# Kernel tuning notes

Measured on AMD Instinct MI355X. Metric: run time of the kernel, lower is better.

Reference implementation:

```python
import jax, jax.numpy as jnp
import numpy as np

D = 1024
H = 16
DH = D // H
FF = 4096
EPS = 1e-6


def setup_inputs() -> dict:
    key = jax.random.key(0)
    ks = jax.random.split(key, 8)
    s = 1.0 / np.sqrt(D)
    return {
        "x": jax.random.normal(ks[0], (2, 2048, D), jnp.float32),
        # attention projections stored [in, out] (math equals torch Linear x @ W.T)
        "w_q": jax.random.normal(ks[1], (D, D), jnp.float32) * s,
        "w_k": jax.random.normal(ks[2], (D, D), jnp.float32) * s,
        "w_v": jax.random.normal(ks[3], (D, D), jnp.float32) * s,
        "w_o": jax.random.normal(ks[4], (D, D), jnp.float32) * s,
        "w1": jax.random.normal(ks[5], (D, FF), jnp.float32) * s,
        "b1": jnp.zeros((FF,), jnp.float32),
        "w2": jax.random.normal(ks[6], (FF, D), jnp.float32) * (1.0 / np.sqrt(FF)),
        "b2": jnp.zeros((D,), jnp.float32),
        "g1": jnp.ones((D,), jnp.float32),
        "be1": jnp.zeros((D,), jnp.float32),
        "g2": jnp.ones((D,), jnp.float32),
        "be2": jnp.zeros((D,), jnp.float32),
    }


def _layernorm(x, gamma, beta):
    # torch .std() uses Bessel correction (ddof=1); note std+eps, not var+eps
    mean = jnp.mean(x, axis=-1, keepdims=True)
    std = jnp.std(x, axis=-1, keepdims=True, ddof=1)
    return gamma * (x - mean) / (std + EPS) + beta


def _attention(h, w_q, w_k, w_v, w_o):
    B, S, _ = h.shape
    q = (h @ w_q).reshape(B, S, H, DH)
    k = (h @ w_k).reshape(B, S, H, DH)
    v = (h @ w_v).reshape(B, S, H, DH)
    scores = jnp.einsum('bqhd,bkhd->bhqk', q, k) / np.sqrt(DH)  # [B,H,S,S]
    attn = jax.nn.softmax(scores, axis=-1)
    out = jnp.einsum('bhqk,bkhd->bqhd', attn, v).reshape(B, S, D)
    return out @ w_o


def reference(x, w_q, w_k, w_v, w_o, w1, b1, w2, b2, g1, be1, g2, be2):
    # pre-norm residual 1: self-attention (dropout=0 / eval)
    x = x + _attention(_layernorm(x, g1, be1), w_q, w_k, w_v, w_o)
    # pre-norm residual 2: FFN
    h = _layernorm(x, g2, be2)
    x = x + (jax.nn.relu(h @ w1 + b1) @ w2 + b2)
    return x
```

## Files before the change

kernel.cpp:

```cpp
#include <hip/hip_runtime.h>


typedef _Float16 half8 __attribute__((ext_vector_type(8)));
typedef _Float16 half4 __attribute__((ext_vector_type(4)));
typedef float floatx4 __attribute__((ext_vector_type(4)));

__device__ __forceinline__ void async16(const void* g, void* l) {
    __builtin_amdgcn_global_load_lds((const __attribute__((address_space(1))) unsigned int*)g,
                                     (__attribute__((address_space(3))) unsigned int*)l,
                                     16, 0, 0);
}

__global__ __launch_bounds__(256) void ln_kernel(const float* __restrict__ x,
                                                 const float* __restrict__ g,
                                                 const float* __restrict__ be,
                                                 _Float16* __restrict__ out) {
    int row = blockIdx.x;
    int tid = threadIdx.x;
    floatx4 v = ((const floatx4*)(x + (size_t)row * 1024))[tid];
    float s = 0.f, ss = 0.f;
#pragma unroll
    for (int i = 0; i < 4; i++) { s += v[i]; ss += v[i] * v[i]; }
#pragma unroll
    for (int off = 1; off < 64; off <<= 1) {
        s += __shfl_xor(s, off);
        ss += __shfl_xor(ss, off);
    }
    __shared__ float sm[8];
    int wave = tid >> 6, lane = tid & 63;
    if (lane == 0) { sm[wave] = s; sm[wave + 4] = ss; }
    __syncthreads();
    s = sm[0] + sm[1] + sm[2] + sm[3];
    ss = sm[4] + sm[5] + sm[6] + sm[7];
    float mean = s * (1.f / 1024.f);
    float var = (ss - s * mean) * (1.f / 1023.f);
    float rs = 1.f / (sqrtf(fmaxf(var, 0.f)) + 1e-6f);
    floatx4 gv = ((const floatx4*)g)[tid];
    floatx4 bv = ((const floatx4*)be)[tid];
    half4 o;
#pragma unroll
    for (int i = 0; i < 4; i++) o[i] = (_Float16)(gv[i] * (v[i] - mean) * rs + bv[i]);
    ((half4*)(out + (size_t)row * 1024))[tid] = o;
}

__global__ __launch_bounds__(256) void convt_kernel(const float* __restrict__ W, int ldW,
                                                    _Float16* __restrict__ WT, int Kr,
                                                    float scale) {
    __shared__ float t[64][65];
    int n0 = blockIdx.x * 64, k0 = blockIdx.y * 64;
    int tid = threadIdx.x;
    int r = tid >> 4, c4 = (tid & 15) * 4;
#pragma unroll
    for (int p = 0; p < 4; p++) {
        floatx4 v = *(const floatx4*)(W + (size_t)(k0 + r + p * 16) * ldW + n0 + c4);
#pragma unroll
        for (int j = 0; j < 4; j++) t[c4 + j][r + p * 16] = v[j];
    }
    __syncthreads();
#pragma unroll
    for (int p = 0; p < 4; p++) {
        int rr = r + p * 16;
        half4 o;
#pragma unroll
        for (int j = 0; j < 4; j++) o[j] = (_Float16)(t[rr][c4 + j] * scale);
        *(half4*)(WT + (size_t)(n0 + rr) * Kr + k0 + c4) = o;
    }
}

__global__ __launch_bounds__(256) void transv_kernel(const _Float16* __restrict__ V, int ldv,
                                                     _Float16* __restrict__ Vt) {
    __shared__ _Float16 t[64][72];
    int t0 = blockIdx.x * 64, d0 = blockIdx.y * 64;
    int tid = threadIdx.x;
#pragma unroll
    for (int i = 0; i < 2; i++) {
        int v = tid + i * 256;
        int r = v >> 3, c = (v & 7) * 8;
        half8 vv = *(const half8*)(V + (size_t)(t0 + r) * ldv + d0 + c);
#pragma unroll
        for (int j = 0; j < 8; j++) t[c + j][r] = vv[j];
    }
    __syncthreads();
    int bh = (t0 >> 11) * 16 + (d0 >> 6);
    int sbase = t0 & 2047;
#pragma unroll
    for (int i = 0; i < 2; i++) {
        int v = tid + i * 256;
        int r = v >> 3, c = (v & 7) * 8;
        half8 o = *(const half8*)&t[r][c];
        *(half8*)(Vt + ((size_t)bh * 64 + r) * 2048 + sbase + c) = o;
    }
}

__global__ __launch_bounds__(256) void gemm_t(const _Float16* __restrict__ A, int lda,
                                              const _Float16* __restrict__ BT,
                                              const float* __restrict__ bias,
                                              const float* res, void* Cout,
                                              int N, int K, int relu_flag, int out_fp16) {
    __shared__ _Float16 As[64 * 64];
    __shared__ _Float16 Bs[128 * 64];
    int tid = threadIdx.x;
    int wave = tid >> 6, lane = tid & 63, quad = lane >> 4, l15 = lane & 15;
    int bm = blockIdx.y * 64, bn = blockIdx.x * 128;
    int wr = (wave & 1) * 32, wc = (wave >> 1) * 64;
    int lrow = lane >> 3, lch = lane & 7;

    floatx4 acc[2][4];
#pragma unroll
    for (int im = 0; im < 2; im++)
#pragma unroll
        for (int in = 0; in < 4; in++)
#pragma unroll
            for (int r = 0; r < 4; r++) acc[im][in][r] = 0.f;

    for (int k0 = 0; k0 < K; k0 += 64) {
        __syncthreads();
#pragma unroll
        for (int ia = 0; ia < 2; ia++) {
            int g = 2 * wave + ia;
            int row = g * 8 + lrow;
            int ch = lch ^ (row & 7);
            async16(A + (size_t)(bm + row) * lda + k0 + ch * 8, &As[g * 512]);
        }
#pragma unroll
        for (int ib = 0; ib < 4; ib++) {
            int g = 4 * wave + ib;
            int row = g * 8 + lrow;
            int ch = lch ^ (row & 7);
            async16(BT + (size_t)(bn + row) * K + k0 + ch * 8, &Bs[g * 512]);
        }
        __syncthreads();

        half8 af[2][2], bf[4][2];
#pragma unroll
        for (int kk = 0; kk < 2; kk++) {
#pragma unroll
            for (int im = 0; im < 2; im++) {
                int m = wr + im * 16 + l15;
                af[im][kk] = *(const half8*)&As[m * 64 + ((((kk << 2) | quad) ^ (m & 7)) << 3)];
            }
#pragma unroll
            for (int in = 0; in < 4; in++) {
                int n = wc + in * 16 + l15;
                bf[in][kk] = *(const half8*)&Bs[n * 64 + ((((kk << 2) | quad) ^ (n & 7)) << 3)];
            }
        }
#pragma unroll
        for (int kk = 0; kk < 2; kk++)
#pragma unroll
            for (int im = 0; im < 2; im++)
#pragma unroll
                for (int in = 0; in < 4; in++)
                    acc[im][in] = __builtin_amdgcn_mfma_f32_16x16x32_f16(af[im][kk], bf[in][kk],
                                                                         acc[im][in], 0, 0, 0);
    }
#pragma unroll
    for (int im = 0; im < 2; im++)
#pragma unroll
        for (int in = 0; in < 4; in++)
#pragma unroll
            for (int r = 0; r < 4; r++) {
                int row = bm + wr + im * 16 + quad * 4 + r;
                int col = bn + wc + in * 16 + l15;
                float val = acc[im][in][r];
                if (bias) val += bias[col];
                if (relu_flag) val = fmaxf(val, 0.f);
                if (res) val += res[(size_t)row * N + col];
                if (out_fp16) ((_Float16*)Cout)[(size_t)row * N + col] = (_Float16)val;
                else          ((float*)Cout)[(size_t)row * N + col] = val;
            }
}

__global__ __launch_bounds__(256) void attn_kernel(const _Float16* Q,
                                                   const _Float16* __restrict__ K,
                                                   const _Float16* __restrict__ Vt,
                                                   _Float16* O, int ld) {
    __shared__ _Float16 Qs[64 * 64];
    __shared__ _Float16 KVs[2][2][64 * 64];
    int qt = blockIdx.x, bh = blockIdx.y;
    int b = bh >> 4, h = bh & 15;
    int col0 = h * 64, tbase = b * 2048;
    int tid = threadIdx.x;
    int wave = tid >> 6, lane = tid & 63, quad = lane >> 4, l15 = lane & 15;
    int lrow = lane >> 3, lch = lane & 7;

#pragma unroll
    for (int i = 0; i < 2; i++) {
        int g = 2 * wave + i;
        int row = g * 8 + lrow;
        int ch = lch ^ (row & 7);
        async16(Q + (size_t)(tbase + qt * 64 + row) * ld + col0 + ch * 8, &Qs[g * 512]);
        async16(K + (size_t)(tbase + row) * ld + col0 + ch * 8, &KVs[0][0][g * 512]);
        async16(Vt + ((size_t)bh * 64 + row) * 2048 + ch * 8, &KVs[0][1][g * 512]);
    }
    __syncthreads();

    int rowq = 16 * wave + l15;
    half8 bq[2];
#pragma unroll
    for (int kk = 0; kk < 2; kk++)
        bq[kk] = *(const half8*)&Qs[rowq * 64 + ((((kk << 2) | quad) ^ (rowq & 7)) << 3)];

    floatx4 o_acc[4];
#pragma unroll
    for (int im = 0; im < 4; im++)
#pragma unroll
        for (int r = 0; r < 4; r++) o_acc[im][r] = 0.f;
    float m_i = -1e30f, l_i = 0.f;

    for (int kt = 0; kt < 32; kt++) {
        if (kt) __syncthreads();
        if (kt + 1 < 32) {
            int nb = (kt + 1) & 1;
#pragma unroll
            for (int i = 0; i < 2; i++) {
                int g = 2 * wave + i;
                int row = g * 8 + lrow;
                int ch = lch ^ (row & 7);
                async16(K + (size_t)(tbase + (kt + 1) * 64 + row) * ld + col0 + ch * 8,
                        &KVs[nb][0][g * 512]);
                async16(Vt + ((size_t)bh * 64 + row) * 2048 + (kt + 1) * 64 + ch * 8,
                        &KVs[nb][1][g * 512]);
            }
        }
        const _Float16* Ks = KVs[kt & 1][0];
        const _Float16* Vs = KVs[kt & 1][1];

        floatx4 s_acc[4];
#pragma unroll
        for (int jn = 0; jn < 4; jn++)
#pragma unroll
            for (int r = 0; r < 4; r++) s_acc[jn][r] = 0.f;
#pragma unroll
        for (int jn = 0; jn < 4; jn++) {
            int rowk = 16 * jn + l15;
#pragma unroll
            for (int kk = 0; kk < 2; kk++) {
                half8 ak = *(const half8*)&Ks[rowk * 64 + ((((kk << 2) | quad) ^ (rowk & 7)) << 3)];
                s_acc[jn] = __builtin_amdgcn_mfma_f32_16x16x32_f16(ak, bq[kk], s_acc[jn], 0, 0, 0);
            }
        }

        float mx = -1e30f;
#pragma unroll
        for (int jn = 0; jn < 4; jn++)
#pragma unroll
            for (int r = 0; r < 4; r++) mx = fmaxf(mx, s_acc[jn][r]);
        mx = fmaxf(mx, __shfl_xor(mx, 16));
        mx = fmaxf(mx, __shfl_xor(mx, 32));
        float mnew = fmaxf(m_i, mx);
        float dd = m_i - mnew;
        float alpha = (dd < -60.f) ? 0.f : __expf(dd);
        m_i = mnew;

        float sum = 0.f;
#pragma unroll
        for (int jn = 0; jn < 4; jn++)
#pragma unroll
            for (int r = 0; r < 4; r++) {
                float d2 = s_acc[jn][r] - mnew;
                float p = (d2 < -60.f) ? 0.f : __expf(d2);
                s_acc[jn][r] = p;
                sum += p;
            }
        sum += __shfl_xor(sum, 16);
        sum += __shfl_xor(sum, 32);
        l_i = l_i * alpha + sum;

        half4 pb[4];
#pragma unroll
        for (int jn = 0; jn < 4; jn++)
#pragma unroll
            for (int r = 0; r < 4; r++) pb[jn][r] = (_Float16)s_acc[jn][r];

#pragma unroll
        for (int im = 0; im < 4; im++)
#pragma unroll
            for (int r = 0; r < 4; r++) o_acc[im][r] *= alpha;
#pragma unroll
        for (int im = 0; im < 4; im++) {
            int rowv = 16 * im + l15;
#pragma unroll
            for (int ks = 0; ks < 4; ks++) {
                int off = rowv * 128 + ((((2 * ks) | (quad >> 1)) ^ (rowv & 7)) << 4) + (quad & 1) * 8;
                half4 av = *(const half4*)((const char*)Vs + off);
                o_acc[im] = __builtin_amdgcn_mfma_f32_16x16x16f16(av, pb[ks], o_acc[im], 0, 0, 0);
            }
        }
    }

    float rl = 1.f / l_i;
#pragma unroll
    for (int im = 0; im < 4; im++) {
        half4 o;
#pragma unroll
        for (int r = 0; r < 4; r++) o[r] = (_Float16)(o_acc[im][r] * rl);
        *(half4*)&O[(size_t)(tbase + qt * 64 + wave * 16 + l15) * ld + col0 + im * 16 + quad * 4] = o;
    }
}

extern "C" void kernel_launch(void* const* d_in, const int* in_sizes, int n_in,
                              void* d_out, int out_size, void* d_ws, size_t ws_size,
                              hipStream_t stream) {
    const float* x   = (const float*)d_in[0];
    const float* wq  = (const float*)d_in[1];
    const float* wk  = (const float*)d_in[2];
    const float* wv  = (const float*)d_in[3];
    const float* wo  = (const float*)d_in[4];
    const float* w1  = (const float*)d_in[5];
    const float* b1  = (const float*)d_in[6];
    const float* w2  = (const float*)d_in[7];
    const float* b2  = (const float*)d_in[8];
    const float* g1  = (const float*)d_in[9];
    const float* be1 = (const float*)d_in[10];
    const float* g2  = (const float*)d_in[11];
    const float* be2 = (const float*)d_in[12];

    const size_t M1 = (size_t)1 << 20;
    _Float16* R0  = (_Float16*)d_ws;
    _Float16* QKV = R0 + 4 * M1;
    _Float16* R3  = R0 + 12 * M1;

    _Float16* wqkvT = (_Float16*)d_out;
    float* x1 = (float*)d_out;
    float* out = (float*)d_out;

    dim3 blk(256);

    convt_kernel<<<dim3(16, 16), blk, 0, stream>>>(wq, 1024, wqkvT, 1024, 0.125f);
    convt_kernel<<<dim3(16, 16), blk, 0, stream>>>(wk, 1024, wqkvT + (size_t)1024 * 1024, 1024, 1.f);
    convt_kernel<<<dim3(16, 16), blk, 0, stream>>>(wv, 1024, wqkvT + (size_t)2048 * 1024, 1024, 1.f);
    ln_kernel<<<4096, blk, 0, stream>>>(x, g1, be1, R0);
    gemm_t<<<dim3(24, 64), blk, 0, stream>>>(R0, 1024, wqkvT, nullptr, nullptr, QKV, 3072, 1024, 0, 1);
    transv_kernel<<<dim3(64, 16), blk, 0, stream>>>(QKV + 2048, 3072, R0);
    attn_kernel<<<dim3(32, 32), blk, 0, stream>>>(QKV, QKV + 1024, R0, QKV, 3072);
    convt_kernel<<<dim3(16, 16), blk, 0, stream>>>(wo, 1024, R0, 1024, 1.f);
    gemm_t<<<dim3(8, 64), blk, 0, stream>>>(QKV, 3072, R0, nullptr, x, x1, 1024, 1024, 0, 0);
    ln_kernel<<<4096, blk, 0, stream>>>(x1, g2, be2, R0);
    _Float16* f = QKV;
    for (int hh = 0; hh < 2; hh++) {
        _Float16* w1Th = R3;
        _Float16* w2Th = R3 + 2 * M1;
        convt_kernel<<<dim3(32, 16), blk, 0, stream>>>(w1 + hh * 2048, 4096, w1Th, 1024, 1.f);
        gemm_t<<<dim3(16, 64), blk, 0, stream>>>(R0, 1024, w1Th, b1 + hh * 2048, nullptr, f,
                                                 2048, 1024, 1, 1);
        convt_kernel<<<dim3(16, 32), blk, 0, stream>>>(w2 + (size_t)hh * 2048 * 1024, 1024, w2Th, 2048, 1.f);
        gemm_t<<<dim3(8, 64), blk, 0, stream>>>(f, 2048, w2Th, (hh == 1) ? b2 : nullptr, x1, out,
                                                1024, 2048, 0, 0);
    }
}
```

Baseline: 441.2 us.

## Add 128x128 GEMM tile, single-buffer attention, exp2 softmax with packed conversion

Adds a 128x128-tile GEMM variant where each wave computes a 64x64 sub-tile, and uses it for the QKV and FFN1 projections to get more register-level reuse and fewer blocks. The attention kernel drops its double-buffered K/V prefetch in favour of a single buffer loaded synchronously each iteration. It also folds log2(e) into the Q scale so softmax can use exp2 without the underflow guard, and converts P to fp16 with packed round-toward-zero. Losing the K/V prefetch exposes load latency, but the halved LDS footprint may allow more blocks per CU.

Result: slower. 452.2 us (+2.5%).

```diff
diff --git a/kernel.cpp b/kernel.cpp
--- a/kernel.cpp
+++ b/kernel.cpp
@@ -3,6 +3,7 @@
 
 typedef _Float16 half8 __attribute__((ext_vector_type(8)));
 typedef _Float16 half4 __attribute__((ext_vector_type(4)));
+typedef __fp16 fp16x2 __attribute__((ext_vector_type(2)));
 typedef float floatx4 __attribute__((ext_vector_type(4)));
 
 __device__ __forceinline__ void async16(const void* g, void* l) {
@@ -92,11 +93,11 @@
     }
 }
 
-__global__ __launch_bounds__(256) void gemm_t(const _Float16* __restrict__ A, int lda,
-                                              const _Float16* __restrict__ BT,
-                                              const float* __restrict__ bias,
-                                              const float* res, void* Cout,
-                                              int N, int K, int relu_flag, int out_fp16) {
+__global__ __launch_bounds__(256) void gemm_t64(const _Float16* __restrict__ A, int lda,
+                                                const _Float16* __restrict__ BT,
+                                                const float* __restrict__ bias,
+                                                const float* res, void* Cout,
+                                                int N, int K, int relu_flag, int out_fp16) {
     __shared__ _Float16 As[64 * 64];
     __shared__ _Float16 Bs[128 * 64];
     int tid = threadIdx.x;
@@ -171,12 +172,92 @@
             }
 }
 
+__global__ __launch_bounds__(256) void gemm_t128(const _Float16* __restrict__ A, int lda,
+                                                 const _Float16* __restrict__ BT,
+                                                 const float* __restrict__ bias,
+                                                 const float* res, void* Cout,
+                                                 int N, int K, int relu_flag, int out_fp16) {
+    __shared__ _Float16 As[128 * 64];
+    __shared__ _Float16 Bs[128 * 64];
+    int tid = threadIdx.x;
+    int wave = tid >> 6, lane = tid & 63, quad = lane >> 4, l15 = lane & 15;
+    int bm = blockIdx.y * 128, bn = blockIdx.x * 128;
+    int wm = (wave >> 1) * 64, wn = (wave & 1) * 64;
+    int lrow = lane >> 3, lch = lane & 7;
+
+    floatx4 acc[4][4];
+#pragma unroll
+    for (int im = 0; im < 4; im++)
+#pragma unroll
+        for (int in = 0; in < 4; in++)
+#pragma unroll
+            for (int r = 0; r < 4; r++) acc[im][in][r] = 0.f;
+
+    for (int k0 = 0; k0 < K; k0 += 64) {
+        __syncthreads();
+#pragma unroll
+        for (int ia = 0; ia < 4; ia++) {
+            int g = 4 * wave + ia;
+            int row = g * 8 + lrow;
+            int ch = lch ^ (row & 7);
+            async16(A + (size_t)(bm + row) * lda + k0 + ch * 8, &As[g * 512]);
+        }
+#pragma unroll
+        for (int ib = 0; ib < 4; ib++) {
+            int g = 4 * wave + ib;
+            int row = g * 8 + lrow;
+            int ch = lch ^ (row & 7);
+            async16(BT + (size_t)(bn + row) * K + k0 + ch * 8, &Bs[g * 512]);
+        }
+        __syncthreads();
+
+        half8 af[4][2], bf[4][2];
+#pragma unroll
+        for (int kk = 0; kk < 2; kk++) {
+#pragma unroll
+            for (int im = 0; im < 4; im++) {
+                int m = wm + im * 16 + l15;
+                af[im][kk] = *(const half8*)&As[m * 64 + ((((kk << 2) | quad) ^ (m & 7)) << 3)];
+            }
+#pragma unroll
+            for (int in = 0; in < 4; in++) {
+                int n = wn + in * 16 + l15;
+                bf[in][kk] = *(const half8*)&Bs[n * 64 + ((((kk << 2) | quad) ^ (n & 7)) << 3)];
+            }
+        }
+#pragma unroll
+        for (int kk = 0; kk < 2; kk++)
+#pragma unroll
+            for (int im = 0; im < 4; im++)
+#pragma unroll
+                for (int in = 0; in < 4; in++)
+                    acc[im][in] = __builtin_amdgcn_mfma_f32_16x16x32_f16(af[im][kk], bf[in][kk],
+                                                                         acc[im][in], 0, 0, 0);
+    }
+#pragma unroll
+    for (int im = 0; im < 4; im++)
+#pragma unroll
+        for (int in = 0; in < 4; in++)
+#pragma unroll
+            for (int r = 0; r < 4; r++) {
+                int row = bm + wm + im * 16 + quad * 4 + r;
+                int col = bn + wn + in * 16 + l15;
+                float val = acc[im][in][r];
+                if (bias) val += bias[col];
+                if (relu_flag) val = fmaxf(val, 0.f);
+                if (res) val += res[(size_t)row * N + col];
+                if (out_fp16) ((_Float16*)Cout)[(size_t)row * N + col] = (_Float16)val;
+                else          ((float*)Cout)[(size_t)row * N + col] = val;
+            }
+}
+
 __global__ __launch_bounds__(256) void attn_kernel(const _Float16* Q,
                                                    const _Float16* __restrict__ K,
                                                    const _Float16* __restrict__ Vt,
                                                    _Float16* O, int ld) {
     __shared__ _Float16 Qs[64 * 64];
-    __shared__ _Float16 KVs[2][2][64 * 64];
+    __shared__ _Float16 Ks[64 * 64];
+    __shared__ _Float16 Vs[64 * 64];
     int qt = blockIdx.x, bh = blockIdx.y;
     int b = bh >> 4, h = bh & 15;
     int col0 = h * 64, tbase = b * 2048;
@@ -190,11 +271,8 @@
         int row = g * 8 + lrow;
         int ch = lch ^ (row & 7);
         async16(Q + (size_t)(tbase + qt * 64 + row) * ld + col0 + ch * 8, &Qs[g * 512]);
-        async16(K + (size_t)(tbase + row) * ld + col0 + ch * 8, &KVs[0][0][g * 512]);
-        async16(Vt + ((size_t)bh * 64 + row) * 2048 + ch * 8, &KVs[0][1][g * 512]);
     }
     __syncthreads();
-
     int rowq = 16 * wave + l15;
     half8 bq[2];
 #pragma unroll
@@ -209,22 +287,16 @@
     float m_i = -1e30f, l_i = 0.f;
 
     for (int kt = 0; kt < 32; kt++) {
-        if (kt) __syncthreads();
-        if (kt + 1 < 32) {
-            int nb = (kt + 1) & 1;
-#pragma unroll
-            for (int i = 0; i < 2; i++) {
-                int g = 2 * wave + i;
-                int row = g * 8 + lrow;
-                int ch = lch ^ (row & 7);
-                async16(K + (size_t)(tbase + (kt + 1) * 64 + row) * ld + col0 + ch * 8,
-                        &KVs[nb][0][g * 512]);
-                async16(Vt + ((size_t)bh * 64 + row) * 2048 + (kt + 1) * 64 + ch * 8,
-                        &KVs[nb][1][g * 512]);
-            }
-        }
-        const _Float16* Ks = KVs[kt & 1][0];
-        const _Float16* Vs = KVs[kt & 1][1];
+        __syncthreads();
+#pragma unroll
+        for (int i = 0; i < 2; i++) {
+            int g = 2 * wave + i;
+            int row = g * 8 + lrow;
+            int ch = lch ^ (row & 7);
+            async16(K + (size_t)(tbase + kt * 64 + row) * ld + col0 + ch * 8, &Ks[g * 512]);
+            async16(Vt + ((size_t)bh * 64 + row) * 2048 + kt * 64 + ch * 8, &Vs[g * 512]);
+        }
+        __syncthreads();
 
         floatx4 s_acc[4];
 #pragma unroll
@@ -249,8 +321,7 @@
         mx = fmaxf(mx, __shfl_xor(mx, 16));
         mx = fmaxf(mx, __shfl_xor(mx, 32));
         float mnew = fmaxf(m_i, mx);
-        float dd = m_i - mnew;
-        float alpha = (dd < -60.f) ? 0.f : __expf(dd);
+        float alpha = __builtin_amdgcn_exp2f(m_i - mnew);
         m_i = mnew;
 
         float sum = 0.f;
@@ -258,8 +329,7 @@
         for (int jn = 0; jn < 4; jn++)
 #pragma unroll
             for (int r = 0; r < 4; r++) {
-                float d2 = s_acc[jn][r] - mnew;
-                float p = (d2 < -60.f) ? 0.f : __expf(d2);
+                float p = __builtin_amdgcn_exp2f(s_acc[jn][r] - mnew);
                 s_acc[jn][r] = p;
                 sum += p;
             }
@@ -269,9 +339,12 @@
 
         half4 pb[4];
 #pragma unroll
-        for (int jn = 0; jn < 4; jn++)
-#pragma unroll
-            for (int r = 0; r < 4; r++) pb[jn][r] = (_Float16)s_acc[jn][r];
+        for (int jn = 0; jn < 4; jn++) {
+            fp16x2 lo = __builtin_amdgcn_cvt_pkrtz(s_acc[jn][0], s_acc[jn][1]);
+            fp16x2 hi = __builtin_amdgcn_cvt_pkrtz(s_acc[jn][2], s_acc[jn][3]);
+            pb[jn][0] = (_Float16)lo[0]; pb[jn][1] = (_Float16)lo[1];
+            pb[jn][2] = (_Float16)hi[0]; pb[jn][3] = (_Float16)hi[1];
+        }
 
 #pragma unroll
         for (int im = 0; im < 4; im++)
@@ -327,25 +400,25 @@
 
     dim3 blk(256);
 
-    convt_kernel<<<dim3(16, 16), blk, 0, stream>>>(wq, 1024, wqkvT, 1024, 0.125f);
+    convt_kernel<<<dim3(16, 16), blk, 0, stream>>>(wq, 1024, wqkvT, 1024, 0.125f * 1.44269504f);
     convt_kernel<<<dim3(16, 16), blk, 0, stream>>>(wk, 1024, wqkvT + (size_t)1024 * 1024, 1024, 1.f);
     convt_kernel<<<dim3(16, 16), blk, 0, stream>>>(wv, 1024, wqkvT + (size_t)2048 * 1024, 1024, 1.f);
     ln_kernel<<<4096, blk, 0, stream>>>(x, g1, be1, R0);
-    gemm_t<<<dim3(24, 64), blk, 0, stream>>>(R0, 1024, wqkvT, nullptr, nullptr, QKV, 3072, 1024, 0, 1);
+    gemm_t128<<<dim3(24, 32), blk, 0, stream>>>(R0, 1024, wqkvT, nullptr, nullptr, QKV, 3072, 1024, 0, 1);
     transv_kernel<<<dim3(64, 16), blk, 0, stream>>>(QKV + 2048, 3072, R0);
     attn_kernel<<<dim3(32, 32), blk, 0, stream>>>(QKV, QKV + 1024, R0, QKV, 3072);
     convt_kernel<<<dim3(16, 16), blk, 0, stream>>>(wo, 1024, R0, 1024, 1.f);
-    gemm_t<<<dim3(8, 64), blk, 0, stream>>>(QKV, 3072, R0, nullptr, x, x1, 1024, 1024, 0, 0);
+    gemm_t64<<<dim3(8, 64), blk, 0, stream>>>(QKV, 3072, R0, nullptr, x, x1, 1024, 1024, 0, 0);
     ln_kernel<<<4096, blk, 0, stream>>>(x1, g2, be2, R0);
     _Float16* f = QKV;
     for (int hh = 0; hh < 2; hh++) {
         _Float16* w1Th = R3;
         _Float16* w2Th = R3 + 2 * M1;
         convt_kernel<<<dim3(32, 16), blk, 0, stream>>>(w1 + hh * 2048, 4096, w1Th, 1024, 1.f);
-        gemm_t<<<dim3(16, 64), blk, 0, stream>>>(R0, 1024, w1Th, b1 + hh * 2048, nullptr, f,
-                                                 2048, 1024, 1, 1);
+        gemm_t128<<<dim3(16, 32), blk, 0, stream>>>(R0, 1024, w1Th, b1 + hh * 2048, nullptr, f,
+                                                    2048, 1024, 1, 1);
         convt_kernel<<<dim3(16, 32), blk, 0, stream>>>(w2 + (size_t)hh * 2048 * 1024, 1024, w2Th, 2048, 1.f);
-        gemm_t<<<dim3(8, 64), blk, 0, stream>>>(f, 2048, w2Th, (hh == 1) ? b2 : nullptr, x1, out,
-                                                1024, 2048, 0, 0);
-    }
-}
+        gemm_t64<<<dim3(8, 64), blk, 0, stream>>>(f, 2048, w2Th, (hh == 1) ? b2 : nullptr, x1, out,
+                                                  1024, 2048, 0, 0);
+    }
+}
```
